# Kernel optimization log

Hardware: AMD Instinct MI355X
Metric: run time of the kernel (lower is better)

Reference implementation:

```python
import jax, jax.numpy as jnp
import numpy as np

PERCENTAGE = 0.26
BN_EPS = 1e-5


def _conv1x1(x, w, b):
    # x: (B,C,H,W), w: (O,C), b: (O,)
    return jnp.einsum('bchw,oc->bohw', x, w) + b[None, :, None, None]


def _bn_train(x, gamma, beta):
    # BatchNorm2d in training mode: biased variance over (B,H,W) per channel
    mean = x.mean(axis=(0, 2, 3), keepdims=True)
    var = jnp.mean((x - mean) ** 2, axis=(0, 2, 3), keepdims=True)
    xhat = (x - mean) * jax.lax.rsqrt(var + BN_EPS)
    return xhat * gamma[None, :, None, None] + beta[None, :, None, None]


def _band_mask(w, max_w):
    # The two mask-construction loops in the torch code reduce to |i-j| < max_w
    idx = jnp.arange(w)
    return jnp.abs(idx[:, None] - idx[None, :]) < max_w  # (w, w) bool


def setup_inputs() -> dict:
    key = jax.random.key(0)
    ks = jax.random.split(key, 16)
    B, C, H, W = 2, 256, 64, 512
    s = 0.02  # weight scale to keep attention logits in a sane range
    return {
        'x1': jax.random.normal(ks[0], (B, C, H, W), jnp.float32),
        'x2': jax.random.normal(ks[1], (B, C, H, W), jnp.float32),
        'Qw': jax.random.normal(ks[2], (C, C), jnp.float32) * s,
        'Qb': jax.random.normal(ks[3], (C,), jnp.float32) * s,
        'Kw': jax.random.normal(ks[4], (C, C), jnp.float32) * s,
        'Kb': jax.random.normal(ks[5], (C,), jnp.float32) * s,
        'Vw': jax.random.normal(ks[6], (C, C), jnp.float32) * s,
        'Vb': jax.random.normal(ks[7], (C,), jnp.float32) * s,
        'Vg': jax.random.normal(ks[8], (C,), jnp.float32),
        'Vbeta': jax.random.normal(ks[9], (C,), jnp.float32),
        'Ww': jax.random.normal(ks[10], (C, C), jnp.float32) * s,
        'Wb': jax.random.normal(ks[11], (C,), jnp.float32) * s,
        'Wg': jax.random.normal(ks[12], (C,), jnp.float32),
        'Wbeta': jax.random.normal(ks[13], (C,), jnp.float32),
    }


def reference(x1, x2, Qw, Qb, Kw, Kb, Vw, Vb, Vg, Vbeta, Ww, Wb, Wg, Wbeta):
    b, c, h, w = x1.shape
    max_w = int(w * PERCENTAGE)
    mask = _band_mask(w, max_w)  # (w, w), broadcasts over (b*h) rows
    neg_inf = jnp.float32(-jnp.inf)

    def rows(x):  # (B,C,H,W) -> (B*H, W, C)
        return x.transpose(0, 2, 3, 1).reshape(b * h, w, c)

    q1 = rows(_conv1x1(x1, Qw, Qb))
    q2 = rows(_conv1x1(x2, Qw, Qb))
    k1 = rows(_conv1x1(x1, Kw, Kb))  # (B*H, W, C); contract over C below
    k2 = rows(_conv1x1(x2, Kw, Kb))
    v1 = rows(_bn_train(_conv1x1(x1, Vw, Vb), Vg, Vbeta))
    v2 = rows(_bn_train(_conv1x1(x2, Vw, Vb), Vg, Vbeta))

    def attend(q, k, v):
        scores = jnp.einsum('nqc,nkc->nqk', q, k)  # (B*H, W, W)
        scores = jnp.where(mask[None], scores, neg_inf)
        p = jax.nn.softmax(scores, axis=-1)
        return jnp.einsum('nqk,nkc->nqc', p, v)

    def cols(y):  # (B*H, W, C) -> (B,C,H,W)
        return y.reshape(b, h, w, c).transpose(0, 3, 1, 2)

    y1 = cols(attend(q1, k2, v2))
    y2 = cols(attend(q2, k1, v1))
    z1 = _bn_train(_conv1x1(y1, Ww, Wb), Wg, Wbeta) + x1
    z2 = _bn_train(_conv1x1(y2, Ww, Wb), Wg, Wbeta) + x2
    return (z1, z2)
```

## Files before the change

### kernel.cpp

```cpp
#include <hip/hip_runtime.h>

typedef unsigned short u16;
typedef short bfrag __attribute__((ext_vector_type(8)));
typedef float ffrag __attribute__((ext_vector_type(4)));
typedef u16 u16x4 __attribute__((ext_vector_type(4)));

#define MFMA16(a,b,c) __builtin_amdgcn_mfma_f32_16x16x32_bf16((a),(b),(c),0,0,0)

#define WAITV(N) do { asm volatile("s_waitcnt vmcnt(" #N ")" ::: "memory"); \
                      __builtin_amdgcn_sched_barrier(0); } while(0)
#define RBAR()   do { __builtin_amdgcn_s_barrier(); \
                      __builtin_amdgcn_sched_barrier(0); } while(0)


__device__ __forceinline__ u16 f2bf(float f){
  union { float f; unsigned int i; } cv; cv.f = f;
  unsigned int x = cv.i;
  return (u16)((x + 0x7fffu + ((x >> 16) & 1u)) >> 16);
}
__device__ __forceinline__ float bf2f(u16 u){
  union { unsigned int i; float f; } cv;
  cv.i = ((unsigned int)u) << 16;
  return cv.f;
}
__device__ __forceinline__ unsigned cvtpk(float lo, float hi){
  unsigned r; asm("v_cvt_pk_bf16_f32 %0, %1, %2" : "=v"(r) : "v"(lo), "v"(hi)); return r;
}
__device__ __forceinline__ bfrag ldb(const u16* p){
  bfrag v; __builtin_memcpy(&v, p, 16); return v;
}
__device__ __forceinline__ void gload_lds16(const u16* g, u16* l){
  __builtin_amdgcn_global_load_lds(
      (const __attribute__((address_space(1))) unsigned int*)g,
      (__attribute__((address_space(3))) unsigned int*)l, 16, 0, 0);
}

__global__ __launch_bounds__(256) void k_wcvt(const float* __restrict__ qw, const float* __restrict__ kw,
                                              const float* __restrict__ vw, const float* __restrict__ ww,
                                              u16* __restrict__ out){
  int t = blockIdx.x*256 + threadIdx.x;
  out[t]        = f2bf(qw[t]);
  out[t+65536]  = f2bf(kw[t]);
  out[t+131072] = f2bf(vw[t]);
  out[t+196608] = f2bf(ww[t]);
}

__global__ __launch_bounds__(256) void k_xpose(const float* __restrict__ x1, const float* __restrict__ x2,
                                               u16* __restrict__ xr1, u16* __restrict__ xr2){
  const float* x = blockIdx.z ? x2 : x1;
  u16* xr = blockIdx.z ? xr2 : xr1;
  __shared__ float T[64][65];
  int t = threadIdx.x;
  int p0 = blockIdx.x*64, c0 = blockIdx.y*64;
  int b = p0 >> 15, q0 = p0 & 32767;
  #pragma unroll
  for (int it=0; it<4; ++it){
    int cc = it*16 + (t>>4);
    int pi = (t&15)*4;
    ffrag v; __builtin_memcpy(&v, x + ((size_t)(b*256 + c0 + cc))*32768 + q0 + pi, 16);
    T[cc][pi+0]=v[0]; T[cc][pi+1]=v[1]; T[cc][pi+2]=v[2]; T[cc][pi+3]=v[3];
  }
  __syncthreads();
  int pi = t>>2, cj0 = (t&3)*16;
  u16 tmp[16];
  #pragma unroll
  for (int j=0;j<16;++j) tmp[j] = f2bf(T[cj0+j][pi]);
  __builtin_memcpy(xr + (size_t)(p0+pi)*256 + c0 + cj0, tmp, 32);
}

__device__ __forceinline__ void stage_tile(const u16* __restrict__ src, int row0, int k0,
                                           u16* lds, int wid, int l){
  #pragma unroll
  for (int rr=0; rr<4; ++rr){
    int off = rr*4096 + wid*1024 + l*16;
    int row = off>>7, inb = off&127;
    int srcb = inb ^ ((row&7)<<4);
    gload_lds16(src + (size_t)(row0+row)*256 + k0 + (srcb>>1),
                lds + ((rr*4096 + wid*1024)>>1));
  }
}

__global__ __launch_bounds__(256, 2) void k_qkv(const u16* __restrict__ xr1, const u16* __restrict__ xr2,
    const u16* __restrict__ wb,
    const float* __restrict__ qb, const float* __restrict__ kb, const float* __restrict__ vb,
    u16* __restrict__ Q1, u16* __restrict__ K1, u16* __restrict__ V1,
    u16* __restrict__ Q2, u16* __restrict__ K2, u16* __restrict__ V2){
  __shared__ __align__(16) u16 As[2][8192];
  __shared__ __align__(16) u16 Bs[2][8192];
  int id = blockIdx.x;
  int xcd = id & 7, j = id >> 3;
  int pl = j/12, v = j - pl*12;
  int ptile = xcd*64 + pl;
  int ot = v & 1, r = v >> 1;
  int wgt = r >> 1, s = r & 1;
  const u16* A = s ? xr2 : xr1;
  const u16* W = wb + wgt*65536;
  const float* bias = (wgt==0)? qb : (wgt==1)? kb : vb;

  int t = threadIdx.x, wid = t>>6, l = t&63, lr = l&15, lg = l>>4;
  int p0 = ptile*128, o0 = ot*128;
  int wr = (wid>>1)*64, wc = (wid&1)*64;
  int swz = (lr&7)<<4;

  stage_tile(A, p0, 0,  As[0], wid, l);
  stage_tile(W, o0, 0,  Bs[0], wid, l);
  stage_tile(A, p0, 64, As[1], wid, l);
  stage_tile(W, o0, 64, Bs[1], wid, l);

  const ffrag fz = {0.f,0.f,0.f,0.f};
  ffrag acc[4][4];
  #pragma unroll
  for (int i=0;i<4;++i){ acc[i][0]=fz; acc[i][1]=fz; acc[i][2]=fz; acc[i][3]=fz; }

  #pragma unroll
  for (int ks=0; ks<4; ++ks){
    if (ks < 3) { WAITV(8); } else { WAITV(0); }
    RBAR();
    const u16* as = As[ks&1];
    const u16* bs = Bs[ks&1];
    #pragma unroll
    for (int kc=0; kc<2; ++kc){
      int colb = (kc*64 + lg*16) ^ swz;
      bfrag af[4], bfm[4];
      #pragma unroll
      for (int mt=0; mt<4; ++mt)
        af[mt] = ldb(as + (((wr + mt*16 + lr)*128 + colb)>>1));
      #pragma unroll
      for (int nt=0; nt<4; ++nt)
        bfm[nt] = ldb(bs + (((wc + nt*16 + lr)*128 + colb)>>1));
      #pragma unroll
      for (int mt=0; mt<4; ++mt)
        #pragma unroll
        for (int nt=0; nt<4; ++nt)
          acc[mt][nt] = MFMA16(af[mt], bfm[nt], acc[mt][nt]);
    }
    RBAR();
    if (ks < 2){
      stage_tile(A, p0, (ks+2)*64, As[ks&1], wid, l);
      stage_tile(W, o0, (ks+2)*64, Bs[ks&1], wid, l);
    }
  }

  u16* Qo = s ? Q2 : Q1;
  u16* Ko = s ? K2 : K1;
  u16* Vt = s ? V2 : V1;
  #pragma unroll
  for (int nt=0; nt<4; ++nt){
    int oo = o0 + wc + nt*16 + lr;
    float bsc = bias[oo];
    #pragma unroll
    for (int mt=0; mt<4; ++mt){
      int pr = p0 + wr + mt*16 + lg*4;
      if (wgt == 2){
        int n = pr >> 9, w0 = pr & 511;
        u16x4 vv;
        #pragma unroll
        for (int rr=0;rr<4;++rr) vv[rr] = f2bf(acc[mt][nt][rr] + bsc);
        *reinterpret_cast<u16x4*>(Vt + ((size_t)(n*256 + oo))*512 + w0) = vv;
      } else {
        u16* op = (wgt==0)? Qo : Ko;
        #pragma unroll
        for (int rr=0;rr<4;++rr)
          op[(size_t)(pr + rr)*256 + oo] = f2bf(acc[mt][nt][rr] + bsc);
      }
    }
  }
}

__global__ __launch_bounds__(256, 2) void k_conv1(const u16* __restrict__ in1, const u16* __restrict__ in2,
    const u16* __restrict__ wp, const float* __restrict__ bias,
    u16* __restrict__ o1, u16* __restrict__ o2,
    float* __restrict__ psum, float* __restrict__ psq){
  __shared__ __align__(16) u16 As[2][8192];
  __shared__ __align__(16) u16 Bs[2][8192];
  int id = blockIdx.x;
  int xcd = id & 7, j = id >> 3;
  int pl = j>>2, v = j&3;
  int ptile = xcd*64 + pl;
  int ot = v & 1, s = v >> 1;
  const u16* A = s ? in2 : in1;
  u16* out = s ? o2 : o1;

  int t = threadIdx.x, wid = t>>6, l = t&63, lr = l&15, lg = l>>4;
  int p0 = ptile*128, o0 = ot*128;
  int wr = (wid>>1)*64, wc = (wid&1)*64;
  int swz = (lr&7)<<4;

  stage_tile(A, p0, 0,  As[0], wid, l);
  stage_tile(wp, o0, 0, Bs[0], wid, l);
  stage_tile(A, p0, 64, As[1], wid, l);
  stage_tile(wp, o0, 64,Bs[1], wid, l);

  const ffrag fz = {0.f,0.f,0.f,0.f};
  ffrag acc[4][4];
  #pragma unroll
  for (int i=0;i<4;++i){ acc[i][0]=fz; acc[i][1]=fz; acc[i][2]=fz; acc[i][3]=fz; }

  #pragma unroll
  for (int ks=0; ks<4; ++ks){
    if (ks < 3) { WAITV(8); } else { WAITV(0); }
    RBAR();
    const u16* as = As[ks&1];
    const u16* bs = Bs[ks&1];
    #pragma unroll
    for (int kc=0; kc<2; ++kc){
      int colb = (kc*64 + lg*16) ^ swz;
      bfrag af[4], bfm[4];
      #pragma unroll
      for (int mt=0; mt<4; ++mt)
        af[mt] = ldb(as + (((wr + mt*16 + lr)*128 + colb)>>1));
      #pragma unroll
      for (int nt=0; nt<4; ++nt)
        bfm[nt] = ldb(bs + (((wc + nt*16 + lr)*128 + colb)>>1));
      #pragma unroll
      for (int mt=0; mt<4; ++mt)
        #pragma unroll
        for (int nt=0; nt<4; ++nt)
          acc[mt][nt] = MFMA16(af[mt], bfm[nt], acc[mt][nt]);
    }
    RBAR();
    if (ks < 2){
      stage_tile(A, p0, (ks+2)*64, As[ks&1], wid, l);
      stage_tile(wp, o0, (ks+2)*64, Bs[ks&1], wid, l);
    }
  }

  float pv[4], qv[4];
  #pragma unroll
  for (int nt=0; nt<4; ++nt){ pv[nt]=0.f; qv[nt]=0.f; }
  #pragma unroll
  for (int nt=0; nt<4; ++nt){
    int oo = o0 + wc + nt*16 + lr;
    float bsc = bias[oo];
    #pragma unroll
    for (int mt=0; mt<4; ++mt){
      int pr = p0 + wr + mt*16 + lg*4;
      #pragma unroll
      for (int rr=0;rr<4;++rr){
        float val = acc[mt][nt][rr] + bsc;
        out[(size_t)(pr + rr)*256 + oo] = f2bf(val);
        pv[nt] += val; qv[nt] += val*val;
      }
    }
  }
  #pragma unroll
  for (int nt=0; nt<4; ++nt){
    float sv = pv[nt], sq = qv[nt];
    sv += __shfl_xor(sv,16,64); sv += __shfl_xor(sv,32,64);
    sq += __shfl_xor(sq,16,64); sq += __shfl_xor(sq,32,64);
    if (lg==0){
      int oo = o0 + wc + nt*16 + lr;
      int idx = ((s*256 + oo)<<10) + (ptile<<1) + (wr>>6);
      psum[idx] = sv; psq[idx] = sq;
    }
  }
}

__global__ __launch_bounds__(256) void k_vstat1(const u16* __restrict__ V1, const u16* __restrict__ V2,
                                                float* __restrict__ ps, float* __restrict__ pq){
  int s = blockIdx.z;
  const u16* Vt = s ? V2 : V1;
  int c = blockIdx.x, ch = blockIdx.y, t = threadIdx.x;
  float sm=0.f, sq=0.f;
  for (int nn=0; nn<16; ++nn){
    const u16* row = Vt + ((size_t)((ch*16+nn)*256 + c))*512 + t;
    float v = bf2f(row[0]);   sm+=v; sq+=v*v;
    v = bf2f(row[256]);       sm+=v; sq+=v*v;
  }
  __shared__ float rs[256], rq[256];
  rs[t]=sm; rq[t]=sq; __syncthreads();
  for (int st=128; st>0; st>>=1){ if (t<st){ rs[t]+=rs[t+st]; rq[t]+=rq[t+st]; } __syncthreads(); }
  if (t==0){ ps[s*2048 + c*8+ch]=rs[0]; pq[s*2048 + c*8+ch]=rq[0]; }
}
__global__ __launch_bounds__(256) void k_vstat2(const float* __restrict__ ps, const float* __restrict__ pq,
                                                const float* __restrict__ g, const float* __restrict__ be,
                                                float* __restrict__ aVall, float* __restrict__ bVall){
  int s = blockIdx.x, c = threadIdx.x;
  float sm=0.f, sq=0.f;
  #pragma unroll
  for (int ch=0; ch<8; ++ch){ sm += ps[s*2048 + c*8+ch]; sq += pq[s*2048 + c*8+ch]; }
  float mean = sm*(1.f/65536.f);
  float var  = sq*(1.f/65536.f) - mean*mean;
  float aa = g[c]*rsqrtf(var + 1e-5f);
  aVall[s*256+c]=aa; bVall[s*256+c]=be[c]-aa*mean;
}

__device__ __forceinline__ void stageK(const u16* Kn, u16* kb, int kt, int wid, int l){
  #pragma unroll
  for (int c2=0; c2<2; ++c2){
    int off = wid*2048 + c2*1024 + l*16;
    int row = off>>9, inb = off&511;
    int src = inb ^ ((row&7)<<4);
    gload_lds16(Kn + (size_t)(kt*16+row)*256 + (src>>1), kb + wid*1024 + c2*512);
  }
}
__device__ __forceinline__ void stageV(const u16* Vn, u16* vb, int k0, int wid, int l){
  #pragma unroll
  for (int c4=0; c4<4; ++c4){
    int off = wid*4096 + c4*1024 + l*16;
    int crow = off>>6, slot = (off>>4)&3;
    int kk = slot ^ ((crow>>1)&3);
    gload_lds16(Vn + (size_t)crow*512 + k0 + (kk<<3), vb + ((wid*4096 + c4*1024)>>1));
  }
}

__global__ __launch_bounds__(256, 2) void k_attn(
    const u16* __restrict__ Q1, const u16* __restrict__ K2, const u16* __restrict__ V2,
    const u16* __restrict__ Q2, const u16* __restrict__ K1, const u16* __restrict__ V1,
    const float* __restrict__ aVall, const float* __restrict__ bVall,
    u16* __restrict__ O1, u16* __restrict__ O2){
  __shared__ __align__(16) u16 KP[2][8192];
  __shared__ __align__(16) u16 VBs[2][8192];
  int t = threadIdx.x, wid = t>>6, l = t&63, lr = l&15, lg = l>>4;
  int id = blockIdx.x;
  int s = id >> 10;
  int r0 = id & 1023;
  int xcd = r0 & 7, s5 = r0 >> 3;
  int qb = s5 & 7, n = (xcd<<4) | (s5>>3);
  const u16* Q = s ? Q2 : Q1;
  const u16* K = s ? K1 : K2;
  const u16* V = s ? V1 : V2;
  const float* aV = aVall + (s ? 0 : 256);
  const float* bV = bVall + (s ? 0 : 256);
  u16* O = s ? O2 : O1;

  int q0 = qb*64, q0w = q0 + wid*16;
  int lo = q0 - 132; if (lo < 0) lo = 0;
  int hi = q0 + 195; if (hi > 511) hi = 511;
  int KTLO = (lo>>4) & ~1;
  int KTHI = (hi>>4) | 1;
  int nsteps = (KTHI - KTLO + 2) >> 1;

  const u16* Kn = K + (size_t)n*131072;
  const u16* Vn = V + (size_t)n*131072;

  bfrag qa[8];
  const u16* Qrow = Q + ((size_t)(n*512 + q0w + lr))*256 + lg*8;
  #pragma unroll
  for (int ks=0; ks<8; ++ks) qa[ks] = ldb(Qrow + ks*32);
  WAITV(0);

  stageK(Kn, KP[0],        KTLO+0, wid, l);
  stageK(Kn, KP[0]+4096,   KTLO+1, wid, l);
  stageV(Vn, VBs[0],       KTLO*16 + 0,  wid, l);
  stageK(Kn, KP[1],        KTLO+2, wid, l);
  stageK(Kn, KP[1]+4096,   KTLO+3, wid, l);
  stageV(Vn, VBs[1],       KTLO*16 + 32, wid, l);

  const ffrag fz = {0.f,0.f,0.f,0.f};
  ffrag o[16];
  #pragma unroll
  for (int i=0;i<16;++i) o[i] = fz;
  float lsum = 0.f;
  int q = q0w + lr;
  int s0l = lr + (lg&1)*32;
  bool hi2 = (lg & 2) != 0;
  int vswz = (lg ^ ((lr>>1)&3))<<3;

  #pragma unroll
  for (int sp=0; sp<12; ++sp){
    if (sp < nsteps){
      if (sp < nsteps-1) { WAITV(8); } else { WAITV(0); }
      RBAR();
      const u16* kp = KP[sp&1];
      const u16* vb = VBs[sp&1];

      ffrag sA = fz, sB = fz;
      #pragma unroll
      for (int ks=0; ks<8; ++ks){
        int boff = (ks*64 + lg*16) ^ ((lr&7)<<4);
        bfrag kfA = ldb(kp + ((lr*512 + boff)>>1));
        bfrag kfB = ldb(kp + 4096 + ((lr*512 + boff)>>1));
        sA = MFMA16(kfA, qa[ks], sA);
        sB = MFMA16(kfB, qa[ks], sB);
      }

      int baseA = q + 132 - ((KTLO + 2*sp)*16 + lg*4);
      #pragma unroll
      for (int r=0;r<4;++r){
        bool vA = (unsigned)(baseA - r)      < 265u;
        bool vB = (unsigned)(baseA - r - 16) < 265u;
        float eA = vA ? __expf(sA[r]) : 0.f;
        float eB = vB ? __expf(sB[r]) : 0.f;
        sA[r] = eA; sB[r] = eB; lsum += eA + eB;
      }

      unsigned pk0A = cvtpk(sA[0], sA[1]);
      unsigned pk1A = cvtpk(sA[2], sA[3]);
      unsigned pk0B = cvtpk(sB[0], sB[1]);
      unsigned pk1B = cvtpk(sB[2], sB[3]);
      unsigned a0 = (unsigned)__shfl((int)pk0A, s0l,    64);
      unsigned a1 = (unsigned)__shfl((int)pk1A, s0l,    64);
      unsigned a2 = (unsigned)__shfl((int)pk0A, s0l+16, 64);
      unsigned a3 = (unsigned)__shfl((int)pk1A, s0l+16, 64);
      unsigned b0 = (unsigned)__shfl((int)pk0B, s0l,    64);
      unsigned b1 = (unsigned)__shfl((int)pk1B, s0l,    64);
      unsigned b2 = (unsigned)__shfl((int)pk0B, s0l+16, 64);
      unsigned b3 = (unsigned)__shfl((int)pk1B, s0l+16, 64);
      unsigned pu[4];
      pu[0] = hi2 ? b0 : a0;  pu[1] = hi2 ? b1 : a1;
      pu[2] = hi2 ? b2 : a2;  pu[3] = hi2 ? b3 : a3;
      bfrag pa; __builtin_memcpy(&pa, pu, 16);

      #pragma unroll
      for (int ct=0; ct<16; ++ct){
        bfrag vf = ldb(vb + (ct*16 + lr)*32 + vswz);
        o[ct] = MFMA16(pa, vf, o[ct]);
      }
      RBAR();
      if (sp+2 < nsteps){
        stageK(Kn, KP[sp&1],      KTLO + 2*sp + 4, wid, l);
        stageK(Kn, KP[sp&1]+4096, KTLO + 2*sp + 5, wid, l);
        stageV(Vn, VBs[sp&1],     KTLO*16 + (sp+2)*32, wid, l);
      }
    }
  }

  lsum += __shfl_xor(lsum, 16, 64);
  lsum += __shfl_xor(lsum, 32, 64);
  float rinv = 1.f / lsum;
  float linv[4];
  #pragma unroll
  for (int r=0;r<4;++r) linv[r] = __shfl(rinv, (lg<<2)+r, 64);
  #pragma unroll
  for (int ct=0; ct<16; ++ct){
    int c = ct*16 + lr;
    float av = aV[c], bv = bV[c];
    #pragma unroll
    for (int r=0;r<4;++r)
      O[((size_t)(n*512 + q0w + lg*4 + r))*256 + c] = f2bf(av*(o[ct][r]*linv[r]) + bv);
  }
}

__global__ __launch_bounds__(256) void k_ustat2(const float* __restrict__ psum, const float* __restrict__ psq,
                                                const float* __restrict__ g, const float* __restrict__ be,
                                                float* __restrict__ aWall, float* __restrict__ bWall){
  int c = blockIdx.x, s = blockIdx.y, t = threadIdx.x;
  const float* ps = psum + (((size_t)s*256 + c)<<10);
  const float* pq = psq  + (((size_t)s*256 + c)<<10);
  float sm = ps[t] + ps[t+256] + ps[t+512] + ps[t+768];
  float sq = pq[t] + pq[t+256] + pq[t+512] + pq[t+768];
  __shared__ float rs[256], rq[256];
  rs[t]=sm; rq[t]=sq; __syncthreads();
  for (int st=128; st>0; st>>=1){ if (t<st){ rs[t]+=rs[t+st]; rq[t]+=rq[t+st]; } __syncthreads(); }
  if (t==0){
    float mean = rs[0]*(1.f/65536.f);
    float var  = rq[0]*(1.f/65536.f) - mean*mean;
    float aa = g[c]*rsqrtf(var + 1e-5f);
    aWall[s*256+c]=aa; bWall[s*256+c]=be[c]-aa*mean;
  }
}

__global__ __launch_bounds__(256) void k_final(const u16* __restrict__ u1, const u16* __restrict__ u2,
                                               const u16* __restrict__ xr1, const u16* __restrict__ xr2,
                                               const float* __restrict__ aWall, const float* __restrict__ bWall,
                                               float* __restrict__ z){
  int s = blockIdx.z;
  const u16* u  = s ? u2 : u1;
  const u16* xr = s ? xr2 : xr1;
  const float* aW = aWall + s*256;
  const float* bW = bWall + s*256;
  float* zb = z + (size_t)s*16777216;
  __shared__ u16 Tu[64][66], Tx[64][66];
  int t = threadIdx.x;
  int p0 = blockIdx.x*64, c0 = blockIdx.y*64;
  int b = p0>>15, q0 = p0&32767;
  #pragma unroll
  for (int it=0; it<4; ++it){
    int pi = it*16 + (t>>4);
    int cj = (t&15)*4;
    u16x4 vu; __builtin_memcpy(&vu, u  + (size_t)(p0+pi)*256 + c0 + cj, 8);
    u16x4 vx; __builtin_memcpy(&vx, xr + (size_t)(p0+pi)*256 + c0 + cj, 8);
    *reinterpret_cast<u16x4*>(&Tu[pi][cj]) = vu;
    *reinterpret_cast<u16x4*>(&Tx[pi][cj]) = vx;
  }
  __syncthreads();
  #pragma unroll
  for (int it=0; it<16; ++it){
    int cc = it*4 + (t>>6);
    int qi = t&63;
    size_t addr = ((size_t)(b*256 + c0 + cc))*32768 + q0 + qi;
    zb[addr] = aW[c0+cc]*bf2f(Tu[qi][cc]) + bW[c0+cc] + bf2f(Tx[qi][cc]);
  }
}

extern "C" void kernel_launch(void* const* d_in, const int* in_sizes, int n_in,
                              void* d_out, int out_size, void* d_ws, size_t ws_size,
                              hipStream_t stream) {
  const float* x1  = (const float*)d_in[0];
  const float* x2  = (const float*)d_in[1];
  const float* Qw  = (const float*)d_in[2];
  const float* Qb  = (const float*)d_in[3];
  const float* Kw  = (const float*)d_in[4];
  const float* Kb  = (const float*)d_in[5];
  const float* Vw  = (const float*)d_in[6];
  const float* Vb  = (const float*)d_in[7];
  const float* Vg  = (const float*)d_in[8];
  const float* Vbe = (const float*)d_in[9];
  const float* Ww  = (const float*)d_in[10];
  const float* Wb  = (const float*)d_in[11];
  const float* Wg  = (const float*)d_in[12];
  const float* Wbe = (const float*)d_in[13];

  char* ws = (char*)d_ws;
  const size_t S = 33554432;
  u16* xr1 = (u16*)(ws + 0*S);
  u16* xr2 = (u16*)(ws + 1*S);
  u16* Q1  = (u16*)(ws + 2*S);
  u16* K1  = (u16*)(ws + 3*S);
  u16* Q2  = (u16*)(ws + 4*S);
  u16* K2  = (u16*)(ws + 5*S);
  u16* wb  = (u16*)(ws + 6*S);
  float* vec = (float*)(ws + 6*S + 524288);
  float* aVall = vec;
  float* bVall = vec + 512;
  float* aWall = vec + 1024;
  float* bWall = vec + 1536;
  float* vps   = vec + 2048;
  float* vpq   = vps + 4096;

  char* douts = (char*)d_out;
  u16* Vt1 = (u16*)douts;
  u16* Vt2 = (u16*)(douts + S);
  u16* O1  = (u16*)(douts + 2*S);
  u16* O2  = (u16*)(douts + 3*S);
  float* upsum = (float*)douts;
  float* upsq  = upsum + 524288;
  u16* u1 = Q1;  u16* u2 = K1;
  float* z = (float*)d_out;

  dim3 gt(1024, 4, 2);
  dim3 gv(256, 8, 2);
  dim3 gu2(256, 2);

  k_wcvt<<<256, 256, 0, stream>>>(Qw, Kw, Vw, Ww, wb);
  k_xpose<<<gt, 256, 0, stream>>>(x1, x2, xr1, xr2);
  k_qkv<<<6144, 256, 0, stream>>>(xr1, xr2, wb, Qb, Kb, Vb, Q1, K1, Vt1, Q2, K2, Vt2);
  k_vstat1<<<gv, 256, 0, stream>>>(Vt1, Vt2, vps, vpq);
  k_vstat2<<<2, 256, 0, stream>>>(vps, vpq, Vg, Vbe, aVall, bVall);
  k_attn<<<2048, 256, 0, stream>>>(Q1, K2, Vt2, Q2, K1, Vt1, aVall, bVall, O1, O2);
  k_conv1<<<2048, 256, 0, stream>>>(O1, O2, wb + 196608, Wb, u1, u2, upsum, upsq);
  k_ustat2<<<gu2, 256, 0, stream>>>(upsum, upsq, Wg, Wbe, aWall, bWall);
  k_final<<<gt, 256, 0, stream>>>(u1, u2, xr1, xr2, aWall, bWall, z);
}
```

Before: 354.2 us.

## Shrink 1x1-conv GEMM tiles to 128x64, vectorize stores, atomic BN partials

The QKV and output-projection GEMMs now use 128x64 output tiles, with each wave owning 32 rows. The launch grids double and launch bounds rise to allow three blocks per CU. For the Q/K and conv1 outputs, the MFMA operands are swapped so each lane holds four consecutive channels and can write them as one packed vector store instead of scalar u16 stores. Conv1 BN partial sums are reduced across lanes and combined with atomicAdd into a per-ptile buffer, which needs an extra zeroing kernel. The V-stat kernel also switches to 16-byte vector loads. The trade-offs are more total A-tile loads from global memory, atomic traffic, and one more launch.

```diff
diff --git a/kernel.cpp b/kernel.cpp
--- a/kernel.cpp
+++ b/kernel.cpp
@@ -68,10 +68,11 @@
   __builtin_memcpy(xr + (size_t)(p0+pi)*256 + c0 + cj0, tmp, 32);
 }
 
-__device__ __forceinline__ void stage_tile(const u16* __restrict__ src, int row0, int k0,
-                                           u16* lds, int wid, int l){
-  #pragma unroll
-  for (int rr=0; rr<4; ++rr){
+template<int NI>
+__device__ __forceinline__ void stageT(const u16* __restrict__ src, int row0, int k0,
+                                       u16* lds, int wid, int l){
+  #pragma unroll
+  for (int rr=0; rr<NI; ++rr){
     int off = rr*4096 + wid*1024 + l*16;
     int row = off>>7, inb = off&127;
     int srcb = inb ^ ((row&7)<<4);
@@ -80,180 +81,211 @@
   }
 }
 
-__global__ __launch_bounds__(256, 2) void k_qkv(const u16* __restrict__ xr1, const u16* __restrict__ xr2,
+__global__ __launch_bounds__(256, 3) void k_qkv(const u16* __restrict__ xr1, const u16* __restrict__ xr2,
     const u16* __restrict__ wb,
     const float* __restrict__ qb, const float* __restrict__ kb, const float* __restrict__ vb,
     u16* __restrict__ Q1, u16* __restrict__ K1, u16* __restrict__ V1,
     u16* __restrict__ Q2, u16* __restrict__ K2, u16* __restrict__ V2){
   __shared__ __align__(16) u16 As[2][8192];
-  __shared__ __align__(16) u16 Bs[2][8192];
+  __shared__ __align__(16) u16 Bs[2][4096];
   int id = blockIdx.x;
   int xcd = id & 7, j = id >> 3;
-  int pl = j/12, v = j - pl*12;
+  int pl = j/24, v = j - pl*24;
   int ptile = xcd*64 + pl;
-  int ot = v & 1, r = v >> 1;
+  int ot = v & 3, r = v >> 2;
   int wgt = r >> 1, s = r & 1;
   const u16* A = s ? xr2 : xr1;
   const u16* W = wb + wgt*65536;
   const float* bias = (wgt==0)? qb : (wgt==1)? kb : vb;
 
   int t = threadIdx.x, wid = t>>6, l = t&63, lr = l&15, lg = l>>4;
-  int p0 = ptile*128, o0 = ot*128;
-  int wr = (wid>>1)*64, wc = (wid&1)*64;
+  int p0 = ptile*128, o0 = ot*64;
+  int wr = wid*32;
   int swz = (lr&7)<<4;
 
-  stage_tile(A, p0, 0,  As[0], wid, l);
-  stage_tile(W, o0, 0,  Bs[0], wid, l);
-  stage_tile(A, p0, 64, As[1], wid, l);
-  stage_tile(W, o0, 64, Bs[1], wid, l);
+  stageT<4>(A, p0, 0,  As[0], wid, l);
+  stageT<2>(W, o0, 0,  Bs[0], wid, l);
+  stageT<4>(A, p0, 64, As[1], wid, l);
+  stageT<2>(W, o0, 64, Bs[1], wid, l);
 
   const ffrag fz = {0.f,0.f,0.f,0.f};
-  ffrag acc[4][4];
-  #pragma unroll
-  for (int i=0;i<4;++i){ acc[i][0]=fz; acc[i][1]=fz; acc[i][2]=fz; acc[i][3]=fz; }
+  ffrag acc[2][4];
+  #pragma unroll
+  for (int i=0;i<2;++i){ acc[i][0]=fz; acc[i][1]=fz; acc[i][2]=fz; acc[i][3]=fz; }
 
   #pragma unroll
   for (int ks=0; ks<4; ++ks){
-    if (ks < 3) { WAITV(8); } else { WAITV(0); }
+    if (ks < 3) { WAITV(6); } else { WAITV(0); }
     RBAR();
     const u16* as = As[ks&1];
     const u16* bs = Bs[ks&1];
     #pragma unroll
     for (int kc=0; kc<2; ++kc){
       int colb = (kc*64 + lg*16) ^ swz;
-      bfrag af[4], bfm[4];
-      #pragma unroll
-      for (int mt=0; mt<4; ++mt)
+      bfrag af[2], bf[4];
+      #pragma unroll
+      for (int mt=0; mt<2; ++mt)
         af[mt] = ldb(as + (((wr + mt*16 + lr)*128 + colb)>>1));
       #pragma unroll
       for (int nt=0; nt<4; ++nt)
-        bfm[nt] = ldb(bs + (((wc + nt*16 + lr)*128 + colb)>>1));
-      #pragma unroll
-      for (int mt=0; mt<4; ++mt)
+        bf[nt] = ldb(bs + (((nt*16 + lr)*128 + colb)>>1));
+      if (wgt != 2){
         #pragma unroll
-        for (int nt=0; nt<4; ++nt)
-          acc[mt][nt] = MFMA16(af[mt], bfm[nt], acc[mt][nt]);
+        for (int mt=0; mt<2; ++mt)
+          #pragma unroll
+          for (int nt=0; nt<4; ++nt)
+            acc[mt][nt] = MFMA16(bf[nt], af[mt], acc[mt][nt]);
+      } else {
+        #pragma unroll
+        for (int mt=0; mt<2; ++mt)
+          #pragma unroll
+          for (int nt=0; nt<4; ++nt)
+            acc[mt][nt] = MFMA16(af[mt], bf[nt], acc[mt][nt]);
+      }
     }
     RBAR();
     if (ks < 2){
-      stage_tile(A, p0, (ks+2)*64, As[ks&1], wid, l);
-      stage_tile(W, o0, (ks+2)*64, Bs[ks&1], wid, l);
-    }
-  }
-
-  u16* Qo = s ? Q2 : Q1;
-  u16* Ko = s ? K2 : K1;
-  u16* Vt = s ? V2 : V1;
-  #pragma unroll
-  for (int nt=0; nt<4; ++nt){
-    int oo = o0 + wc + nt*16 + lr;
-    float bsc = bias[oo];
-    #pragma unroll
-    for (int mt=0; mt<4; ++mt){
-      int pr = p0 + wr + mt*16 + lg*4;
-      if (wgt == 2){
+      stageT<4>(A, p0, (ks+2)*64, As[ks&1], wid, l);
+      stageT<2>(W, o0, (ks+2)*64, Bs[ks&1], wid, l);
+    }
+  }
+
+  if (wgt != 2){
+    u16* op = (wgt==0) ? (s ? Q2 : Q1) : (s ? K2 : K1);
+    #pragma unroll
+    for (int nt=0; nt<4; ++nt){
+      int ob = o0 + nt*16 + lg*4;
+      ffrag bv = *reinterpret_cast<const ffrag*>(bias + ob);
+      #pragma unroll
+      for (int mt=0; mt<2; ++mt){
+        int p = p0 + wr + mt*16 + lr;
+        u16x4 vv;
+        #pragma unroll
+        for (int rr=0;rr<4;++rr) vv[rr] = f2bf(acc[mt][nt][rr] + bv[rr]);
+        *reinterpret_cast<u16x4*>(op + (size_t)p*256 + ob) = vv;
+      }
+    }
+  } else {
+    u16* Vt = s ? V2 : V1;
+    #pragma unroll
+    for (int nt=0; nt<4; ++nt){
+      int oo = o0 + nt*16 + lr;
+      float bsc = bias[oo];
+      #pragma unroll
+      for (int mt=0; mt<2; ++mt){
+        int pr = p0 + wr + mt*16 + lg*4;
         int n = pr >> 9, w0 = pr & 511;
         u16x4 vv;
         #pragma unroll
         for (int rr=0;rr<4;++rr) vv[rr] = f2bf(acc[mt][nt][rr] + bsc);
         *reinterpret_cast<u16x4*>(Vt + ((size_t)(n*256 + oo))*512 + w0) = vv;
-      } else {
-        u16* op = (wgt==0)? Qo : Ko;
-        #pragma unroll
-        for (int rr=0;rr<4;++rr)
-          op[(size_t)(pr + rr)*256 + oo] = f2bf(acc[mt][nt][rr] + bsc);
-      }
-    }
-  }
-}
-
-__global__ __launch_bounds__(256, 2) void k_conv1(const u16* __restrict__ in1, const u16* __restrict__ in2,
+      }
+    }
+  }
+}
+
+__global__ __launch_bounds__(256, 3) void k_conv1(const u16* __restrict__ in1, const u16* __restrict__ in2,
     const u16* __restrict__ wp, const float* __restrict__ bias,
     u16* __restrict__ o1, u16* __restrict__ o2,
     float* __restrict__ psum, float* __restrict__ psq){
   __shared__ __align__(16) u16 As[2][8192];
-  __shared__ __align__(16) u16 Bs[2][8192];
+  __shared__ __align__(16) u16 Bs[2][4096];
   int id = blockIdx.x;
   int xcd = id & 7, j = id >> 3;
-  int pl = j>>2, v = j&3;
+  int pl = j>>3, v = j&7;
   int ptile = xcd*64 + pl;
-  int ot = v & 1, s = v >> 1;
+  int ot = v & 3, s = v >> 2;
   const u16* A = s ? in2 : in1;
   u16* out = s ? o2 : o1;
 
   int t = threadIdx.x, wid = t>>6, l = t&63, lr = l&15, lg = l>>4;
-  int p0 = ptile*128, o0 = ot*128;
-  int wr = (wid>>1)*64, wc = (wid&1)*64;
+  int p0 = ptile*128, o0 = ot*64;
+  int wr = wid*32;
   int swz = (lr&7)<<4;
 
-  stage_tile(A, p0, 0,  As[0], wid, l);
-  stage_tile(wp, o0, 0, Bs[0], wid, l);
-  stage_tile(A, p0, 64, As[1], wid, l);
-  stage_tile(wp, o0, 64,Bs[1], wid, l);
+  stageT<4>(A, p0, 0,  As[0], wid, l);
+  stageT<2>(wp, o0, 0, Bs[0], wid, l);
+  stageT<4>(A, p0, 64, As[1], wid, l);
+  stageT<2>(wp, o0, 64,Bs[1], wid, l);
 
   const ffrag fz = {0.f,0.f,0.f,0.f};
-  ffrag acc[4][4];
-  #pragma unroll
-  for (int i=0;i<4;++i){ acc[i][0]=fz; acc[i][1]=fz; acc[i][2]=fz; acc[i][3]=fz; }
+  ffrag acc[2][4];
+  #pragma unroll
+  for (int i=0;i<2;++i){ acc[i][0]=fz; acc[i][1]=fz; acc[i][2]=fz; acc[i][3]=fz; }
 
   #pragma unroll
   for (int ks=0; ks<4; ++ks){
-    if (ks < 3) { WAITV(8); } else { WAITV(0); }
+    if (ks < 3) { WAITV(6); } else { WAITV(0); }
     RBAR();
     const u16* as = As[ks&1];
     const u16* bs = Bs[ks&1];
     #pragma unroll
     for (int kc=0; kc<2; ++kc){
       int colb = (kc*64 + lg*16) ^ swz;
-      bfrag af[4], bfm[4];
-      #pragma unroll
-      for (int mt=0; mt<4; ++mt)
+      bfrag af[2], bf[4];
+      #pragma unroll
+      for (int mt=0; mt<2; ++mt)
         af[mt] = ldb(as + (((wr + mt*16 + lr)*128 + colb)>>1));
       #pragma unroll
       for (int nt=0; nt<4; ++nt)
-        bfm[nt] = ldb(bs + (((wc + nt*16 + lr)*128 + colb)>>1));
-      #pragma unroll
-      for (int mt=0; mt<4; ++mt)
+        bf[nt] = ldb(bs + (((nt*16 + lr)*128 + colb)>>1));
+      #pragma unroll
+      for (int mt=0; mt<2; ++mt)
         #pragma unroll
         for (int nt=0; nt<4; ++nt)
-          acc[mt][nt] = MFMA16(af[mt], bfm[nt], acc[mt][nt]);
+          acc[mt][nt] = MFMA16(bf[nt], af[mt], acc[mt][nt]);
     }
     RBAR();
     if (ks < 2){
-      stage_tile(A, p0, (ks+2)*64, As[ks&1], wid, l);
-      stage_tile(wp, o0, (ks+2)*64, Bs[ks&1], wid, l);
-    }
-  }
-
-  float pv[4], qv[4];
-  #pragma unroll
-  for (int nt=0; nt<4; ++nt){ pv[nt]=0.f; qv[nt]=0.f; }
+      stageT<4>(A, p0, (ks+2)*64, As[ks&1], wid, l);
+      stageT<2>(wp, o0, (ks+2)*64, Bs[ks&1], wid, l);
+    }
+  }
+
+  float pv[4][4], qv[4][4];
+  #pragma unroll
+  for (int nt=0; nt<4; ++nt)
+    #pragma unroll
+    for (int rr=0; rr<4; ++rr){ pv[nt][rr]=0.f; qv[nt][rr]=0.f; }
+
   #pragma unroll
   for (int nt=0; nt<4; ++nt){
-    int oo = o0 + wc + nt*16 + lr;
-    float bsc = bias[oo];
-    #pragma unroll
-    for (int mt=0; mt<4; ++mt){
-      int pr = p0 + wr + mt*16 + lg*4;
+    int ob = o0 + nt*16 + lg*4;
+    ffrag bv = *reinterpret_cast<const ffrag*>(bias + ob);
+    #pragma unroll
+    for (int mt=0; mt<2; ++mt){
+      int p = p0 + wr + mt*16 + lr;
+      u16x4 vv;
       #pragma unroll
       for (int rr=0;rr<4;++rr){
-        float val = acc[mt][nt][rr] + bsc;
-        out[(size_t)(pr + rr)*256 + oo] = f2bf(val);
-        pv[nt] += val; qv[nt] += val*val;
-      }
-    }
-  }
-  #pragma unroll
-  for (int nt=0; nt<4; ++nt){
-    float sv = pv[nt], sq = qv[nt];
-    sv += __shfl_xor(sv,16,64); sv += __shfl_xor(sv,32,64);
-    sq += __shfl_xor(sq,16,64); sq += __shfl_xor(sq,32,64);
-    if (lg==0){
-      int oo = o0 + wc + nt*16 + lr;
-      int idx = ((s*256 + oo)<<10) + (ptile<<1) + (wr>>6);
-      psum[idx] = sv; psq[idx] = sq;
-    }
-  }
+        float val = acc[mt][nt][rr] + bv[rr];
+        vv[rr] = f2bf(val);
+        pv[nt][rr] += val; qv[nt][rr] += val*val;
+      }
+      *reinterpret_cast<u16x4*>(out + (size_t)p*256 + ob) = vv;
+    }
+  }
+  #pragma unroll
+  for (int nt=0; nt<4; ++nt)
+    #pragma unroll
+    for (int rr=0; rr<4; ++rr){
+      float sv = pv[nt][rr], sq = qv[nt][rr];
+      sv += __shfl_xor(sv,1,64); sv += __shfl_xor(sv,2,64);
+      sv += __shfl_xor(sv,4,64); sv += __shfl_xor(sv,8,64);
+      sq += __shfl_xor(sq,1,64); sq += __shfl_xor(sq,2,64);
+      sq += __shfl_xor(sq,4,64); sq += __shfl_xor(sq,8,64);
+      if (lr==0){
+        int o = o0 + nt*16 + lg*4 + rr;
+        size_t idx = (((size_t)(s*256 + o))<<9) + ptile;
+        atomicAdd(&psum[idx], sv);
+        atomicAdd(&psq[idx],  sq);
+      }
+    }
+}
+
+__global__ __launch_bounds__(256) void k_zero(float* __restrict__ p, int n){
+  int i = blockIdx.x*256 + threadIdx.x;
+  if (i < n) p[i] = 0.f;
 }
 
 __global__ __launch_bounds__(256) void k_vstat1(const u16* __restrict__ V1, const u16* __restrict__ V2,
@@ -261,11 +293,13 @@
   int s = blockIdx.z;
   const u16* Vt = s ? V2 : V1;
   int c = blockIdx.x, ch = blockIdx.y, t = threadIdx.x;
+  const u16* base = Vt + ((size_t)((ch*16 + (t>>4))*256 + c))*512 + (t&15)*32;
   float sm=0.f, sq=0.f;
-  for (int nn=0; nn<16; ++nn){
-    const u16* row = Vt + ((size_t)((ch*16+nn)*256 + c))*512 + t;
-    float v = bf2f(row[0]);   sm+=v; sq+=v*v;
-    v = bf2f(row[256]);       sm+=v; sq+=v*v;
+  #pragma unroll
+  for (int j=0;j<4;++j){
+    bfrag v = ldb(base + j*8);
+    #pragma unroll
+    for (int e=0;e<8;++e){ float f = bf2f((u16)v[e]); sm+=f; sq+=f*f; }
   }
   __shared__ float rs[256], rq[256];
   rs[t]=sm; rq[t]=sq; __syncthreads();
@@ -436,10 +470,10 @@
                                                 const float* __restrict__ g, const float* __restrict__ be,
                                                 float* __restrict__ aWall, float* __restrict__ bWall){
   int c = blockIdx.x, s = blockIdx.y, t = threadIdx.x;
-  const float* ps = psum + (((size_t)s*256 + c)<<10);
-  const float* pq = psq  + (((size_t)s*256 + c)<<10);
-  float sm = ps[t] + ps[t+256] + ps[t+512] + ps[t+768];
-  float sq = pq[t] + pq[t+256] + pq[t+512] + pq[t+768];
+  const float* ps = psum + (((size_t)(s*256 + c))<<9);
+  const float* pq = psq  + (((size_t)(s*256 + c))<<9);
+  float sm = ps[t] + ps[t+256];
+  float sq = pq[t] + pq[t+256];
   __shared__ float rs[256], rq[256];
   rs[t]=sm; rq[t]=sq; __syncthreads();
   for (int st=128; st>0; st>>=1){ if (t<st){ rs[t]+=rs[t+st]; rq[t]+=rq[t+st]; } __syncthreads(); }
@@ -525,7 +559,7 @@
   u16* O1  = (u16*)(douts + 2*S);
   u16* O2  = (u16*)(douts + 3*S);
   float* upsum = (float*)douts;
-  float* upsq  = upsum + 524288;
+  float* upsq  = upsum + 262144;
   u16* u1 = Q1;  u16* u2 = K1;
   float* z = (float*)d_out;
 
@@ -535,11 +569,12 @@
 
   k_wcvt<<<256, 256, 0, stream>>>(Qw, Kw, Vw, Ww, wb);
   k_xpose<<<gt, 256, 0, stream>>>(x1, x2, xr1, xr2);
-  k_qkv<<<6144, 256, 0, stream>>>(xr1, xr2, wb, Qb, Kb, Vb, Q1, K1, Vt1, Q2, K2, Vt2);
+  k_qkv<<<12288, 256, 0, stream>>>(xr1, xr2, wb, Qb, Kb, Vb, Q1, K1, Vt1, Q2, K2, Vt2);
   k_vstat1<<<gv, 256, 0, stream>>>(Vt1, Vt2, vps, vpq);
   k_vstat2<<<2, 256, 0, stream>>>(vps, vpq, Vg, Vbe, aVall, bVall);
   k_attn<<<2048, 256, 0, stream>>>(Q1, K2, Vt2, Q2, K1, Vt1, aVall, bVall, O1, O2);
-  k_conv1<<<2048, 256, 0, stream>>>(O1, O2, wb + 196608, Wb, u1, u2, upsum, upsq);
+  k_zero<<<2048, 256, 0, stream>>>(upsum, 524288);
+  k_conv1<<<4096, 256, 0, stream>>>(O1, O2, wb + 196608, Wb, u1, u2, upsum, upsq);
   k_ustat2<<<gu2, 256, 0, stream>>>(upsum, upsq, Wg, Wbe, aWall, bWall);
   k_final<<<gt, 256, 0, stream>>>(u1, u2, xr1, xr2, aWall, bWall, z);
 }
```

After: 420.7 us. +18.8%, slower.
